# Optimization experiments

Hardware: AMD Instinct MI355X
Metric: run time of the kernel (lower is better)

## Reference

```python
import jax, jax.numpy as jnp
import numpy as np

# Model dims (mamba_ssm defaults: expand=2, d_state=16, d_conv=4, dt_rank=ceil(d_model/16))
V, D_MODEL, N_LAYERS = 32000, 768, 2
D_INNER, D_STATE, D_CONV, DT_RANK = 1536, 16, 4, 48
BATCH, SEQ = 2, 2048


def setup_inputs() -> dict:
    key = jax.random.key(0)
    ks = jax.random.split(key, 10)

    def nrm(k, shape, s=0.02):
        return (jax.random.normal(k, shape) * s).astype(jnp.float32)

    x = jax.random.randint(ks[0], (BATCH, SEQ), 0, V)
    emb = nrm(ks[1], (V, D_MODEL))
    # per-layer Mamba params, stacked on leading layer axis
    W_in = nrm(ks[2], (N_LAYERS, 2 * D_INNER, D_MODEL))          # in_proj (no bias)
    conv_w = nrm(ks[3], (N_LAYERS, D_INNER, 1, D_CONV), 0.1)      # depthwise causal conv
    conv_b = jnp.zeros((N_LAYERS, D_INNER), jnp.float32)
    W_x = nrm(ks[4], (N_LAYERS, DT_RANK + 2 * D_STATE, D_INNER))  # x_proj (no bias)
    W_dt = nrm(ks[5], (N_LAYERS, D_INNER, DT_RANK), 0.05)         # dt_proj
    b_dt = jnp.full((N_LAYERS, D_INNER), -4.0, jnp.float32)       # softplus(-4) ~ small dt
    # A initialized as -exp(A_log) with A_log = log(1..d_state), per mamba_ssm
    A_log = jnp.log(jnp.broadcast_to(
        jnp.arange(1, D_STATE + 1, dtype=jnp.float32), (N_LAYERS, D_INNER, D_STATE)))
    D_skip = jnp.ones((N_LAYERS, D_INNER), jnp.float32)
    W_out = nrm(ks[6], (N_LAYERS, D_MODEL, D_INNER))              # out_proj (no bias)
    ln_g = jnp.ones((D_MODEL,), jnp.float32)
    ln_b = jnp.zeros((D_MODEL,), jnp.float32)
    head_w = nrm(ks[7], (V, D_MODEL))
    head_b = jnp.zeros((V,), jnp.float32)
    return dict(x=x, emb=emb, W_in=W_in, conv_w=conv_w, conv_b=conv_b, W_x=W_x,
                W_dt=W_dt, b_dt=b_dt, A_log=A_log, D_skip=D_skip, W_out=W_out,
                ln_g=ln_g, ln_b=ln_b, head_w=head_w, head_b=head_b)


def mamba_block(h, W_in, conv_w, conv_b, W_x, W_dt, b_dt, A_log, D_skip, W_out):
    # h: (B, L, D_MODEL)
    xz = jnp.einsum('bld,ed->ble', h, W_in)              # (B, L, 2*d_inner)
    u, z = jnp.split(xz, 2, axis=-1)
    # causal depthwise conv over time
    uc = jnp.transpose(u, (0, 2, 1))                     # (B, d_inner, L)
    uc = jax.lax.conv_general_dilated(
        uc, conv_w, window_strides=(1,), padding=[(D_CONV - 1, 0)],
        feature_group_count=D_INNER, dimension_numbers=('NCH', 'OIH', 'NCH'))
    u = jax.nn.silu(jnp.transpose(uc, (0, 2, 1)) + conv_b)
    # input-dependent dt, B, C
    x_dbl = jnp.einsum('bld,ed->ble', u, W_x)            # (B, L, dt_rank+2*d_state)
    dtl, Bm, Cm = jnp.split(x_dbl, [DT_RANK, DT_RANK + D_STATE], axis=-1)
    dt = jax.nn.softplus(jnp.einsum('blr,dr->bld', dtl, W_dt) + b_dt)  # (B, L, d_inner)
    A = -jnp.exp(A_log)                                  # (d_inner, d_state)

    def step(hst, inp):
        dt_t, u_t, B_t, C_t = inp                        # (B,d_inner),(B,d_inner),(B,d_state),(B,d_state)
        hst = jnp.exp(dt_t[..., None] * A) * hst + (dt_t * u_t)[..., None] * B_t[:, None, :]
        y_t = jnp.einsum('bds,bs->bd', hst, C_t)
        return hst, y_t

    h0 = jnp.zeros((u.shape[0], D_INNER, D_STATE), u.dtype)
    xs = (dt.transpose(1, 0, 2), u.transpose(1, 0, 2),
          Bm.transpose(1, 0, 2), Cm.transpose(1, 0, 2))
    _, ys = jax.lax.scan(step, h0, xs)                   # (L, B, d_inner)
    y = ys.transpose(1, 0, 2) + u * D_skip
    y = y * jax.nn.silu(z)
    return jnp.einsum('bli,oi->blo', y, W_out)           # back to (B, L, D_MODEL)


def reference(x, emb, W_in, conv_w, conv_b, W_x, W_dt, b_dt, A_log, D_skip,
              W_out, ln_g, ln_b, head_w, head_b):
    h = emb[x]                                           # (B, L, D_MODEL)
    for l in range(N_LAYERS):
        h = h + mamba_block(h, W_in[l], conv_w[l], conv_b[l], W_x[l], W_dt[l],
                            b_dt[l], A_log[l], D_skip[l], W_out[l])
    mu = jnp.mean(h, axis=-1, keepdims=True)
    var = jnp.mean((h - mu) ** 2, axis=-1, keepdims=True)
    hn = (h - mu) * jax.lax.rsqrt(var + 1e-5) * ln_g + ln_b
    return jnp.einsum('bld,vd->blv', hn, head_w) + head_b
```

## Files before the change

### kernel.cpp

```cpp
#include <hip/hip_runtime.h>
#include <hip/hip_bf16.h>
#include <stdint.h>

#define BL    4096
#define DM    768
#define DI    1536
#define DS    16
#define DCONV 4
#define DTR   48
#define NL    2
#define SEQL  2048
#define BATCH 2
#define VOC   32000
#define NCH   32
#define CT    64

typedef __bf16 bf16_t;
typedef __bf16 bf16x8 __attribute__((ext_vector_type(8)));
typedef __bf16 bf16x4 __attribute__((ext_vector_type(4)));
typedef float  f32x4  __attribute__((ext_vector_type(4)));

__device__ __forceinline__ float sigmoidf_(float x) { return 1.f / (1.f + __expf(-x)); }
__device__ __forceinline__ float softplus_(float x) {
  return (x > 20.f) ? x : log1pf(__expf(x));
}

__global__ __launch_bounds__(256) void k_embed(const int* __restrict__ x,
                                               const float* __restrict__ emb,
                                               float* __restrict__ h,
                                               bf16_t* __restrict__ hb,
                                               bf16_t* __restrict__ dtl) {
  int row = blockIdx.x;
  if (row < 256) {
    int r = row * 16 + (threadIdx.x >> 4);
    dtl[r * 64 + 48 + (threadIdx.x & 15)] = (bf16_t)0.f;
  }
  int tok = x[row];
  const float* e = emb + (size_t)tok * DM;
  float* hr = h + (size_t)row * DM;
  bf16_t* hbr = hb + (size_t)row * DM;
  for (int c = threadIdx.x; c < DM; c += 256) {
    float v = e[c];
    hr[c] = v;
    hbr[c] = (bf16_t)v;
  }
}

#define NV0 1179648L
#define NV1 589824L
#define NV2 6144000L
#define NS3 393216L
#define NS4 196608L
#define NVT (NV0 + NV1 + NV2)
#define NTOT (NVT + NS3 + NS4)

__global__ __launch_bounds__(256) void k_cvtw(const float* __restrict__ Win,
                                              const float* __restrict__ Wout,
                                              const float* __restrict__ Whead,
                                              const float* __restrict__ Wx,
                                              const float* __restrict__ Wdt,
                                              bf16_t* __restrict__ bin,
                                              bf16_t* __restrict__ bout,
                                              bf16_t* __restrict__ bhead,
                                              bf16_t* __restrict__ bx,
                                              bf16_t* __restrict__ bdt) {
  long i = (long)blockIdx.x * 256 + threadIdx.x;
  if (i >= NTOT) return;
  if (i < NVT) {
    const float* s; bf16_t* d; long j = i;
    if (i < NV0)            { s = Win;   d = bin; }
    else if (i < NV0 + NV1) { s = Wout;  d = bout;  j = i - NV0; }
    else                    { s = Whead; d = bhead; j = i - NV0 - NV1; }
    float4 v = ((const float4*)s)[j];
    bf16x4 o;
    o[0] = (bf16_t)v.x; o[1] = (bf16_t)v.y; o[2] = (bf16_t)v.z; o[3] = (bf16_t)v.w;
    ((bf16x4*)d)[j] = o;
  } else if (i < NVT + NS3) {
    long j = i - NVT;
    int l = (int)(j / (128 * 1536));
    int rr = (int)((j / 1536) % 128);
    int c = (int)(j % 1536);
    bx[j] = (bf16_t)(rr < 80 ? Wx[((long)l * 80 + rr) * 1536 + c] : 0.f);
  } else {
    long j = i - NVT - NS3;
    int l = (int)(j / (1536 * 64));
    int r = (int)((j / 64) % 1536);
    int c = (int)(j & 63);
    bdt[j] = (bf16_t)(c < DTR ? Wdt[((long)l * 1536 + r) * DTR + c] : 0.f);
  }
}

__global__ __launch_bounds__(256) void k_conv(const float* __restrict__ xz,
                                              const float* __restrict__ cw,
                                              const float* __restrict__ cb,
                                              bf16_t* __restrict__ ucb, long total) {
  long i = (long)blockIdx.x * 256 + threadIdx.x;
  if (i >= total) return;
  int d = (int)(i % DI);
  long row = i / DI;
  int l = (int)(row % SEQL);
  const float* w = cw + (size_t)d * DCONV;
  float s = cb[d];
#pragma unroll
  for (int j = 0; j < DCONV; j++) {
    int lj = l - (DCONV - 1) + j;
    if (lj >= 0) s += xz[(row - (DCONV - 1) + j) * (2 * DI) + d] * w[j];
  }
  float v = s * sigmoidf_(s);
  ucb[i] = (bf16_t)v;
}

__global__ __launch_bounds__(256) void k_xfin(const float* __restrict__ xp,
                                              float* __restrict__ xdbl,
                                              bf16_t* __restrict__ dtl) {
  long i = (long)blockIdx.x * 256 + threadIdx.x;
  if (i >= (long)BL * 80) return;
  float s = xp[i] + xp[i + (long)BL * 80] + xp[i + 2L * BL * 80] + xp[i + 3L * BL * 80];
  xdbl[i] = s;
  int row = (int)(i / 80), col = (int)(i % 80);
  if (col < DTR) dtl[(long)row * 64 + col] = (bf16_t)s;
}

__global__ __launch_bounds__(256) void k_scan1(const bf16_t* __restrict__ dt,
                                               const bf16_t* __restrict__ uc,
                                               const float* __restrict__ xdbl,
                                               const float* __restrict__ A_log,
                                               float* __restrict__ cA,
                                               float* __restrict__ cB) {
  int gi = blockIdx.x * 256 + threadIdx.x;
  int s = gi & 15;
  int rest = gi >> 4;
  int d = rest % DI;
  int rest2 = rest / DI;
  int c = rest2 % NCH;
  int b = rest2 / NCH;
  float a = -__expf(A_log[d * DS + s]);
  long l0 = (long)c * CT;
  const bf16_t* dtp = dt + ((long)b * SEQL + l0) * DI + d;
  const bf16_t* ucp = uc + ((long)b * SEQL + l0) * DI + d;
  const float*  Bp  = xdbl + ((long)b * SEQL + l0) * 80 + DTR + s;
  float S = 0.f, hh = 0.f;
#pragma unroll 4
  for (int l = 0; l < CT; l++) {
    float dtv = (float)dtp[(long)l * DI];
    float uv  = (float)ucp[(long)l * DI];
    float Bv  = Bp[(long)l * 80];
    S += dtv;
    hh = __expf(dtv * a) * hh + (dtv * uv) * Bv;
  }
  cA[gi] = __expf(a * S);
  cB[gi] = hh;
}

__global__ __launch_bounds__(256) void k_scan2(const float* __restrict__ cA,
                                               const float* __restrict__ cB,
                                               float* __restrict__ hst) {
  int gj = blockIdx.x * 256 + threadIdx.x;
  int ds_ = gj & (DI * DS - 1);
  int b = gj / (DI * DS);
  float h = 0.f;
#pragma unroll
  for (int c = 0; c < NCH; c++) {
    long idx = ((long)(b * NCH + c) * DI * DS) + ds_;
    hst[idx] = h;
    h = cA[idx] * h + cB[idx];
  }
}

__global__ __launch_bounds__(256) void k_scan3g(const bf16_t* __restrict__ dt,
                                                const bf16_t* uc,
                                                const float* __restrict__ xdbl,
                                                const float* __restrict__ A_log,
                                                const float* __restrict__ hst,
                                                const float* __restrict__ xz,
                                                const float* __restrict__ Dsk,
                                                bf16_t* o) {
  int gi = blockIdx.x * 256 + threadIdx.x;
  int s = gi & 15;
  int rest = gi >> 4;
  int d = rest % DI;
  int rest2 = rest / DI;
  int c = rest2 % NCH;
  int b = rest2 / NCH;
  float a = -__expf(A_log[d * DS + s]);
  float dval = Dsk[d];
  long l0 = (long)c * CT;
  const bf16_t* dtp = dt + ((long)b * SEQL + l0) * DI + d;
  const bf16_t* ucp = uc + ((long)b * SEQL + l0) * DI + d;
  const float*  Bp  = xdbl + ((long)b * SEQL + l0) * 80 + DTR + s;
  const float*  Cp  = Bp + DS;
  const float*  zp  = xz + ((long)b * SEQL + l0) * (2 * DI) + DI + d;
  bf16_t* yp = o + ((long)b * SEQL + l0) * DI + d;
  float h = hst[gi];
#pragma unroll 4
  for (int l = 0; l < CT; l++) {
    float dtv = (float)dtp[(long)l * DI];
    float uv  = (float)ucp[(long)l * DI];
    float Bv  = Bp[(long)l * 80];
    float Cv  = Cp[(long)l * 80];
    h = __expf(dtv * a) * h + (dtv * uv) * Bv;
    float y = h * Cv;
    y += __shfl_xor(y, 1);
    y += __shfl_xor(y, 2);
    y += __shfl_xor(y, 4);
    y += __shfl_xor(y, 8);
    if (s == 0) {
      float z = zp[(long)l * 2 * DI];
      float yy = (y + uv * dval) * z * sigmoidf_(z);
      yp[(long)l * DI] = (bf16_t)yy;
    }
  }
}

__global__ __launch_bounds__(256) void k_ln(const float* __restrict__ h,
                                            const float* __restrict__ g,
                                            const float* __restrict__ bta,
                                            bf16_t* __restrict__ o) {
  __shared__ float sm[4];
  int row = blockIdx.x;
  int t = threadIdx.x;
  const float* hr = h + (long)row * DM;
  float v0 = hr[t], v1 = hr[t + 256], v2 = hr[t + 512];
  float s = v0 + v1 + v2;
#pragma unroll
  for (int off = 32; off > 0; off >>= 1) s += __shfl_down(s, off);
  if ((t & 63) == 0) sm[t >> 6] = s;
  __syncthreads();
  float mu = (sm[0] + sm[1] + sm[2] + sm[3]) * (1.f / DM);
  __syncthreads();
  float d0 = v0 - mu, d1 = v1 - mu, d2 = v2 - mu;
  float q = d0 * d0 + d1 * d1 + d2 * d2;
#pragma unroll
  for (int off = 32; off > 0; off >>= 1) q += __shfl_down(q, off);
  if ((t & 63) == 0) sm[t >> 6] = q;
  __syncthreads();
  float var = (sm[0] + sm[1] + sm[2] + sm[3]) * (1.f / DM);
  float rs = rsqrtf(var + 1e-5f);
  bf16_t* orow = o + (long)row * DM;
  orow[t]       = (bf16_t)(d0 * rs * g[t]       + bta[t]);
  orow[t + 256] = (bf16_t)(d1 * rs * g[t + 256] + bta[t + 256]);
  orow[t + 512] = (bf16_t)(d2 * rs * g[t + 512] + bta[t + 512]);
}

__device__ __forceinline__ void stage16(const bf16_t* gp, bf16_t* lp) {
  __builtin_amdgcn_global_load_lds(
      (const __attribute__((address_space(1))) uint32_t*)gp,
      (__attribute__((address_space(3))) uint32_t*)lp, 16, 0, 0);
}

#define WAITV8()  asm volatile("s_waitcnt vmcnt(8)" ::: "memory")
#define WAITV0()  asm volatile("s_waitcnt vmcnt(0)" ::: "memory")
#define BARRIER() do { __builtin_amdgcn_s_barrier();                            \
                       asm volatile("" ::: "memory"); } while (0)

#define GLD256(ab, j, ktt, pp) do {                                             \
    int idx_ = (j) * 512 + tid;                                                 \
    int r_ = idx_ >> 3; int c16_ = idx_ & 7;                                    \
    size_t col_ = (size_t)(ktt) * 64 + (size_t)((c16_ ^ (r_ & 7)) << 3);        \
    const bf16_t* gp_ = (ab) ? (Wp + ((size_t)(n0 + r_)) * K + col_)            \
                             : (Ap + ((size_t)(m0 + r_)) * K + col_);           \
    bf16_t* lp_ = lds + ((((pp) * 2 + (ab)) * 256 + r_) * 64) + c16_ * 8;       \
    stage16(gp_, lp_);                                                          \
  } while (0)

#define STAGE256(pp, ktt) do {                                                  \
    GLD256(0, 0, ktt, pp); GLD256(0, 1, ktt, pp);                               \
    GLD256(0, 2, ktt, pp); GLD256(0, 3, ktt, pp);                               \
    GLD256(1, 0, ktt, pp); GLD256(1, 1, ktt, pp);                               \
    GLD256(1, 2, ktt, pp); GLD256(1, 3, ktt, pp);                               \
  } while (0)

#define COMPUTE_KH(pp, kh) do {                                                 \
    const char* lb_ = (const char*)lds;                                         \
    bf16x8 bfr_[4];                                                             \
    _Pragma("unroll") for (int f = 0; f < 4; ++f) {                             \
      int row_ = wn * 64 + f * 16 + fr;                                         \
      int byte_ = (((pp) * 2 + 1) * 256 + row_) * 128 +                         \
                  (((kh) * 64 + kq * 16) ^ ((row_ & 7) << 4));                  \
      bfr_[f] = *(const bf16x8*)(lb_ + byte_);                                  \
    }                                                                           \
    _Pragma("unroll") for (int mg = 0; mg < 2; ++mg) {                          \
      bf16x8 afr_[4];                                                           \
      _Pragma("unroll") for (int f = 0; f < 4; ++f) {                           \
        int row_ = wm * 128 + mg * 64 + f * 16 + fr;                            \
        int byte_ = (((pp) * 2 + 0) * 256 + row_) * 128 +                       \
                    (((kh) * 64 + kq * 16) ^ ((row_ & 7) << 4));                \
        afr_[f] = *(const bf16x8*)(lb_ + byte_);                                \
      }                                                                         \
      __builtin_amdgcn_s_setprio(1);                                            \
      _Pragma("unroll") for (int fm = 0; fm < 4; ++fm)                          \
        _Pragma("unroll") for (int fn = 0; fn < 4; ++fn)                        \
          acc[mg * 4 + fm][fn] = __builtin_amdgcn_mfma_f32_16x16x32_bf16(       \
              afr_[fm], bfr_[fn], acc[mg * 4 + fm][fn], 0, 0, 0);               \
      __builtin_amdgcn_s_setprio(0);                                            \
    }                                                                           \
  } while (0)

template <int EPI>
__global__ __launch_bounds__(512, 2) void k_gemm256(const bf16_t* __restrict__ Ap,
                                                    const bf16_t* __restrict__ Wp,
                                                    float* __restrict__ C,
                                                    const float* __restrict__ bias,
                                                    int K, int ldc) {
  __shared__ bf16_t lds[2 * 2 * 256 * 64];
  const int tid = threadIdx.x;
  const int lane = tid & 63;
  const int wid = tid >> 6;
  const int wm = wid >> 2, wn = wid & 3;
  const int fr = lane & 15, kq = lane >> 4;

  const int cpx = gridDim.x >> 3;
  const int wg = ((int)blockIdx.x & 7) * cpx + ((int)blockIdx.x >> 3);
  const long m0 = (long)(wg & 15) * 256;
  const long n0 = (long)(wg >> 4) * 256;

  f32x4 acc[8][4];
#pragma unroll
  for (int i = 0; i < 8; i++)
#pragma unroll
    for (int j = 0; j < 4; j++) acc[i][j] = (f32x4){0.f, 0.f, 0.f, 0.f};

  STAGE256(0, 0);
  const int NT = K >> 6;
  for (int kt = 0; kt < NT; ++kt) {
    const int p = kt & 1;
    const bool pre = (kt + 1 < NT);
    if (pre) STAGE256(p ^ 1, kt + 1);
    if (pre) WAITV8(); else WAITV0();
    BARRIER();
    COMPUTE_KH(p, 0);
    COMPUTE_KH(p, 1);
    BARRIER();
  }

  {
    float* lf = (float*)(void*)lds;
    const int q = lane >> 4;
    const int cc = lane & 15;
    float4 bias4 = {0.f, 0.f, 0.f, 0.f};
    if (EPI == 1) bias4 = *(const float4*)&bias[n0 + lane * 4];
#pragma unroll
    for (int p = 0; p < 4; ++p) {
      __syncthreads();
      if (wm == (p >> 1)) {
        const int mgb = (p & 1) * 4;
#pragma unroll
        for (int m4 = 0; m4 < 4; ++m4)
#pragma unroll
          for (int n = 0; n < 4; ++n) {
            f32x4 v = acc[mgb + m4][n];
            float* dst = &lf[(m4 * 16 + q * 4) * 260 + wn * 64 + n * 16 + cc];
#pragma unroll
            for (int r = 0; r < 4; ++r) dst[r * 260] = v[r];
          }
      }
      __syncthreads();
      const long rowg0 = m0 + p * 64;
#pragma unroll
      for (int it = 0; it < 8; ++it) {
        int row_loc = wid * 8 + it;
        f32x4 v = *(const f32x4*)&lf[row_loc * 260 + lane * 4];
        float* gp = &C[(rowg0 + row_loc) * (long)ldc + n0 + lane * 4];
        if (EPI == 1) {
          v[0] += bias4.x; v[1] += bias4.y; v[2] += bias4.z; v[3] += bias4.w;
          __builtin_nontemporal_store(v, (f32x4*)gp);
        } else {
          *(f32x4*)gp = v;
        }
      }
    }
  }
}

#define GLD128(ab, j, ktt, pp) do {                                             \
    int idx_ = (j) * 256 + tid;                                                 \
    int r_ = idx_ >> 3; int c16_ = idx_ & 7;                                    \
    size_t col_ = kb + (size_t)(ktt) * 64 + (size_t)((c16_ ^ (r_ & 7)) << 3);   \
    const bf16_t* gp_ = (ab) ? (Wp + ((size_t)(n0 + r_)) * K + col_)            \
                             : (Ap + ((size_t)(m0 + r_)) * K + col_);           \
    bf16_t* lp_ = lds + ((((pp) * 2 + (ab)) * 128 + r_) * 64) + c16_ * 8;       \
    stage16(gp_, lp_);                                                          \
  } while (0)

#define STAGE128(pp, ktt) do {                                                  \
    GLD128(0, 0, ktt, pp); GLD128(0, 1, ktt, pp);                               \
    GLD128(0, 2, ktt, pp); GLD128(0, 3, ktt, pp);                               \
    GLD128(1, 0, ktt, pp); GLD128(1, 1, ktt, pp);                               \
    GLD128(1, 2, ktt, pp); GLD128(1, 3, ktt, pp);                               \
  } while (0)

#define COMPUTE128(pp, kh) do {                                                 \
    const char* lb_ = (const char*)lds;                                         \
    bf16x8 af_[4], bv_[4];                                                      \
    _Pragma("unroll") for (int f = 0; f < 4; ++f) {                             \
      int row_ = wn * 64 + f * 16 + fr;                                         \
      int byte_ = (((pp) * 2 + 1) * 128 + row_) * 128 +                         \
                  (((kh) * 64 + kq * 16) ^ ((row_ & 7) << 4));                  \
      bv_[f] = *(const bf16x8*)(lb_ + byte_);                                   \
    }                                                                           \
    _Pragma("unroll") for (int f = 0; f < 4; ++f) {                             \
      int row_ = wm * 64 + f * 16 + fr;                                         \
      int byte_ = (((pp) * 2 + 0) * 128 + row_) * 128 +                         \
                  (((kh) * 64 + kq * 16) ^ ((row_ & 7) << 4));                  \
      af_[f] = *(const bf16x8*)(lb_ + byte_);                                   \
    }                                                                           \
    __builtin_amdgcn_s_setprio(1);                                              \
    _Pragma("unroll") for (int fm = 0; fm < 4; ++fm)                            \
      _Pragma("unroll") for (int fn = 0; fn < 4; ++fn)                          \
        acc[fm][fn] = __builtin_amdgcn_mfma_f32_16x16x32_bf16(                  \
            af_[fm], bv_[fn], acc[fm][fn], 0, 0, 0);                            \
    __builtin_amdgcn_s_setprio(0);                                              \
  } while (0)

template <int EPI>
__global__ __launch_bounds__(256, 2) void k_gemm128(const bf16_t* __restrict__ Ap,
                                                    const bf16_t* __restrict__ Wp,
                                                    float* __restrict__ C,
                                                    const float* __restrict__ bias,
                                                    bf16_t* __restrict__ side,
                                                    int K, int Ksl, int ldc) {
  __shared__ bf16_t lds[2 * 2 * 128 * 64];
  const int tid = threadIdx.x;
  const int lane = tid & 63;
  const int wv = tid >> 6;
  const int wm = wv >> 1, wn = wv & 1;
  const int fr = lane & 15, kq = lane >> 4;
  const size_t kb = (size_t)blockIdx.y * Ksl;

  const int cpx = gridDim.x >> 3;
  const int wg = ((int)blockIdx.x & 7) * cpx + ((int)blockIdx.x >> 3);
  const long m0 = (long)(wg & 31) * 128;
  const long n0 = (long)(wg >> 5) * 128;

  f32x4 acc[4][4];
#pragma unroll
  for (int i = 0; i < 4; i++)
#pragma unroll
    for (int j = 0; j < 4; j++) acc[i][j] = (f32x4){0.f, 0.f, 0.f, 0.f};

  STAGE128(0, 0);
  const int NT = Ksl >> 6;
  for (int kt = 0; kt < NT; ++kt) {
    const int p = kt & 1;
    const bool pre = (kt + 1 < NT);
    if (pre) STAGE128(p ^ 1, kt + 1);
    if (pre) WAITV8(); else WAITV0();
    BARRIER();
    COMPUTE128(p, 0);
    COMPUTE128(p, 1);
    BARRIER();
  }

  if (EPI == 7) {
    float* Cs = C + (size_t)blockIdx.y * (size_t)BL * 80;
    const int r4 = (lane >> 4) * 4;
    const int cc = lane & 15;
#pragma unroll
    for (int fm = 0; fm < 4; fm++) {
      long rowb = m0 + wm * 64 + fm * 16 + r4;
#pragma unroll
      for (int fn = 0; fn < 4; fn++) {
        long col = n0 + wn * 64 + fn * 16 + cc;
        if (col < 80) {
#pragma unroll
          for (int r = 0; r < 4; r++)
            Cs[(rowb + r) * 80 + col] = acc[fm][fn][r];
        }
      }
    }
    return;
  }

  {
    float* lf = (float*)(void*)lds;
    const int q = lane >> 4;
    const int cc = lane & 15;
    const int colt = (tid & 31) * 4;
    float4 bias4 = {0.f, 0.f, 0.f, 0.f};
    if (EPI == 4) bias4 = *(const float4*)&bias[n0 + colt];
#pragma unroll
    for (int p = 0; p < 4; ++p) {
      __syncthreads();
      if (wm == (p >> 1)) {
#pragma unroll
        for (int fl = 0; fl < 2; ++fl) {
          int fm = (p & 1) * 2 + fl;
#pragma unroll
          for (int fn = 0; fn < 4; ++fn) {
            f32x4 v = acc[fm][fn];
            float* dst = &lf[(fl * 16 + q * 4) * 132 + wn * 64 + fn * 16 + cc];
#pragma unroll
            for (int r = 0; r < 4; ++r) dst[r * 132] = v[r];
          }
        }
      }
      __syncthreads();
      const long rowg0 = m0 + p * 32;
#pragma unroll
      for (int it = 0; it < 4; ++it) {
        int rl = it * 8 + (tid >> 5);
        f32x4 v = *(const f32x4*)&lf[rl * 132 + colt];
        long row = rowg0 + rl;
        long cg = n0 + colt;
        if (EPI == 4) {
          bf16x4 s4;
          s4[0] = (bf16_t)softplus_(v[0] + bias4.x);
          s4[1] = (bf16_t)softplus_(v[1] + bias4.y);
          s4[2] = (bf16_t)softplus_(v[2] + bias4.z);
          s4[3] = (bf16_t)softplus_(v[3] + bias4.w);
          *(bf16x4*)&side[row * (long)ldc + cg] = s4;
        } else {
          float* gp = &C[row * (long)ldc + cg];
          f32x4 c0 = *(const f32x4*)gp;
          v[0] += c0[0]; v[1] += c0[1]; v[2] += c0[2]; v[3] += c0[3];
          *(f32x4*)gp = v;
          bf16x4 s4;
          s4[0] = (bf16_t)v[0]; s4[1] = (bf16_t)v[1];
          s4[2] = (bf16_t)v[2]; s4[3] = (bf16_t)v[3];
          *(bf16x4*)&side[row * (long)ldc + cg] = s4;
        }
      }
    }
  }
}

static inline int cdiv_l(long a, long b) { return (int)((a + b - 1) / b); }

extern "C" void kernel_launch(void* const* d_in, const int* in_sizes, int n_in,
                              void* d_out, int out_size, void* d_ws, size_t ws_size,
                              hipStream_t stream) {
  (void)in_sizes; (void)n_in; (void)out_size; (void)ws_size;
  const int*   x      = (const int*)  d_in[0];
  const float* emb    = (const float*)d_in[1];
  const float* W_in   = (const float*)d_in[2];
  const float* conv_w = (const float*)d_in[3];
  const float* conv_b = (const float*)d_in[4];
  const float* W_x    = (const float*)d_in[5];
  const float* W_dt   = (const float*)d_in[6];
  const float* b_dt   = (const float*)d_in[7];
  const float* A_log  = (const float*)d_in[8];
  const float* D_skip = (const float*)d_in[9];
  const float* W_out  = (const float*)d_in[10];
  const float* ln_g   = (const float*)d_in[11];
  const float* ln_b   = (const float*)d_in[12];
  const float* head_w = (const float*)d_in[13];
  const float* head_b = (const float*)d_in[14];
  float* out = (float*)d_out;

  bf16_t* abuf   = (bf16_t*)d_ws;
  bf16_t* hbf    = abuf   + (size_t)BL * DI;
  bf16_t* dtl    = hbf    + (size_t)BL * DM;
  bf16_t* wb_in  = dtl    + (size_t)BL * 64;
  bf16_t* wb_out = wb_in  + (size_t)2 * 3072 * 768;
  bf16_t* wb_hd  = wb_out + (size_t)2 * 768 * 1536;
  bf16_t* wb_x   = wb_hd  + (size_t)VOC * DM;
  bf16_t* wb_dt  = wb_x   + (size_t)2 * 128 * 1536;

  float*  xz    = out;
  float*  xdbl  = xz    + (size_t)BL * 2 * DI;
  float*  dtb_f = xdbl  + (size_t)BL * 80;
  bf16_t* dtbb  = (bf16_t*)dtb_f;
  float*  h     = dtb_f + (size_t)BL * DI;
  float*  cA    = h     + (size_t)BL * DM;
  float*  cB    = cA    + (size_t)BATCH * NCH * DI * DS;
  float*  hst   = cB    + (size_t)BATCH * NCH * DI * DS;
  float*  xpart = hst   + (size_t)BATCH * DI * DS;

  const int scan_blocks = BATCH * NCH * DI * DS / 256;
  const int st_blocks   = BATCH * DI * DS / 256;

  k_cvtw<<<cdiv_l(NTOT, 256), 256, 0, stream>>>(W_in, W_out, head_w, W_x, W_dt,
                                                wb_in, wb_out, wb_hd, wb_x, wb_dt);
  k_embed<<<BL, 256, 0, stream>>>(x, emb, h, hbf, dtl);

  for (int l = 0; l < NL; ++l) {
    k_gemm256<0><<<(BL / 256) * (2 * DI / 256), 512, 0, stream>>>(
        hbf, wb_in + (size_t)l * 3072 * 768, xz, nullptr, DM, 2 * DI);
    k_conv<<<cdiv_l((long)BL * DI, 256), 256, 0, stream>>>(
        xz, conv_w + (size_t)l * DI * DCONV, conv_b + (size_t)l * DI,
        abuf, (long)BL * DI);
    k_gemm128<7><<<dim3(32, 4), 256, 0, stream>>>(
        abuf, wb_x + (size_t)l * 128 * 1536, xpart, nullptr, nullptr,
        DI, DI / 4, 80);
    k_xfin<<<cdiv_l((long)BL * 80, 256), 256, 0, stream>>>(xpart, xdbl, dtl);
    k_gemm128<4><<<(BL / 128) * (DI / 128), 256, 0, stream>>>(
        dtl, wb_dt + (size_t)l * 1536 * 64, nullptr, b_dt + (size_t)l * DI, dtbb,
        64, 64, DI);
    k_scan1<<<scan_blocks, 256, 0, stream>>>(dtbb, abuf, xdbl,
                                             A_log + (size_t)l * DI * DS, cA, cB);
    k_scan2<<<st_blocks, 256, 0, stream>>>(cA, cB, hst);
    k_scan3g<<<scan_blocks, 256, 0, stream>>>(dtbb, abuf, xdbl,
                                              A_log + (size_t)l * DI * DS, hst,
                                              xz, D_skip + (size_t)l * DI, abuf);
    k_gemm128<5><<<(BL / 128) * (DM / 128), 256, 0, stream>>>(
        abuf, wb_out + (size_t)l * 768 * 1536, h, nullptr, hbf, DI, DI, DM);
  }

  k_ln<<<BL, 256, 0, stream>>>(h, ln_g, ln_b, abuf);
  k_gemm256<1><<<(BL / 256) * (VOC / 256), 512, 0, stream>>>(
      abuf, wb_hd, out, head_b, DM, VOC);
}
```

Before: 974.7 us.

## Use three-stage K=32 LDS pipeline with packed row layout in 256x256 GEMM

```diff
diff --git a/kernel.cpp b/kernel.cpp
--- a/kernel.cpp
+++ b/kernel.cpp
@@ -249,60 +249,59 @@
 }
 
 #define WAITV8()  asm volatile("s_waitcnt vmcnt(8)" ::: "memory")
+#define WAITV4()  asm volatile("s_waitcnt vmcnt(4)" ::: "memory")
 #define WAITV0()  asm volatile("s_waitcnt vmcnt(0)" ::: "memory")
 #define BARRIER() do { __builtin_amdgcn_s_barrier();                            \
                        asm volatile("" ::: "memory"); } while (0)
 
+
 #define GLD256(ab, j, ktt, pp) do {                                             \
-    int idx_ = (j) * 512 + tid;                                                 \
-    int r_ = idx_ >> 3; int c16_ = idx_ & 7;                                    \
-    size_t col_ = (size_t)(ktt) * 64 + (size_t)((c16_ ^ (r_ & 7)) << 3);        \
+    int L_ = (j) * 512 + tid;                          \
+    int rowp_ = L_ >> 3;                                            \
+    int chs_ = L_ & 7;                                                          \
+    int chl_ = chs_ ^ (rowp_ & 7);                                              \
+    int r_ = rowp_ * 2 + (chl_ >> 2);                                           \
+    size_t col_ = (size_t)(ktt) * 32 + (size_t)((chl_ & 3) * 8);                \
     const bf16_t* gp_ = (ab) ? (Wp + ((size_t)(n0 + r_)) * K + col_)            \
                              : (Ap + ((size_t)(m0 + r_)) * K + col_);           \
-    bf16_t* lp_ = lds + ((((pp) * 2 + (ab)) * 256 + r_) * 64) + c16_ * 8;       \
+    bf16_t* lp_ = lds + ((((pp) * 2 + (ab)) * 128 + rowp_) * 64) + chs_ * 8;    \
     stage16(gp_, lp_);                                                          \
   } while (0)
 
 #define STAGE256(pp, ktt) do {                                                  \
     GLD256(0, 0, ktt, pp); GLD256(0, 1, ktt, pp);                               \
-    GLD256(0, 2, ktt, pp); GLD256(0, 3, ktt, pp);                               \
     GLD256(1, 0, ktt, pp); GLD256(1, 1, ktt, pp);                               \
-    GLD256(1, 2, ktt, pp); GLD256(1, 3, ktt, pp);                               \
   } while (0)
 
-#define COMPUTE_KH(pp, kh) do {                                                 \
+#define FRAG_BYTE(ab, pp, row_)                                                 \
+    ((((pp) * 2 + (ab)) * 128 + ((row_) >> 1)) * 128 +                          \
+     (((((row_) & 1) * 4 + kq) ^ (((row_) >> 1) & 7)) * 16))
+
+#define COMPUTE256(pp) do {                                                     \
     const char* lb_ = (const char*)lds;                                         \
     bf16x8 bfr_[4];                                                             \
     _Pragma("unroll") for (int f = 0; f < 4; ++f) {                             \
       int row_ = wn * 64 + f * 16 + fr;                                         \
-      int byte_ = (((pp) * 2 + 1) * 256 + row_) * 128 +                         \
-                  (((kh) * 64 + kq * 16) ^ ((row_ & 7) << 4));                  \
-      bfr_[f] = *(const bf16x8*)(lb_ + byte_);                                  \
+      bfr_[f] = *(const bf16x8*)(lb_ + FRAG_BYTE(1, pp, row_));                 \
     }                                                                           \
-    _Pragma("unroll") for (int mg = 0; mg < 2; ++mg) {                          \
-      bf16x8 afr_[4];                                                           \
-      _Pragma("unroll") for (int f = 0; f < 4; ++f) {                           \
-        int row_ = wm * 128 + mg * 64 + f * 16 + fr;                            \
-        int byte_ = (((pp) * 2 + 0) * 256 + row_) * 128 +                       \
-                    (((kh) * 64 + kq * 16) ^ ((row_ & 7) << 4));                \
-        afr_[f] = *(const bf16x8*)(lb_ + byte_);                                \
-      }                                                                         \
+    _Pragma("unroll") for (int fm = 0; fm < 8; ++fm) {                          \
+      int row_ = wm * 128 + fm * 16 + fr;                                       \
+      bf16x8 af_ = *(const bf16x8*)(lb_ + FRAG_BYTE(0, pp, row_));              \
       __builtin_amdgcn_s_setprio(1);                                            \
-      _Pragma("unroll") for (int fm = 0; fm < 4; ++fm)                          \
-        _Pragma("unroll") for (int fn = 0; fn < 4; ++fn)                        \
-          acc[mg * 4 + fm][fn] = __builtin_amdgcn_mfma_f32_16x16x32_bf16(       \
-              afr_[fm], bfr_[fn], acc[mg * 4 + fm][fn], 0, 0, 0);               \
+      _Pragma("unroll") for (int fn = 0; fn < 4; ++fn)                          \
+        acc[fm][fn] = __builtin_amdgcn_mfma_f32_16x16x32_bf16(                  \
+            af_, bfr_[fn], acc[fm][fn], 0, 0, 0);                               \
       __builtin_amdgcn_s_setprio(0);                                            \
     }                                                                           \
   } while (0)
 
 template <int EPI>
-__global__ __launch_bounds__(512, 2) void k_gemm256(const bf16_t* __restrict__ Ap,
+__global__ __launch_bounds__(512, 1) void k_gemm256(const bf16_t* __restrict__ Ap,
                                                     const bf16_t* __restrict__ Wp,
                                                     float* __restrict__ C,
                                                     const float* __restrict__ bias,
                                                     int K, int ldc) {
-  __shared__ bf16_t lds[2 * 2 * 256 * 64];
+  __shared__ bf16_t lds[3 * 2 * 128 * 64];
   const int tid = threadIdx.x;
   const int lane = tid & 63;
   const int wid = tid >> 6;
@@ -321,16 +320,23 @@
     for (int j = 0; j < 4; j++) acc[i][j] = (f32x4){0.f, 0.f, 0.f, 0.f};
 
   STAGE256(0, 0);
-  const int NT = K >> 6;
+  STAGE256(1, 1);
+  const int NT = K >> 5;
+  int p = 0;
   for (int kt = 0; kt < NT; ++kt) {
-    const int p = kt & 1;
-    const bool pre = (kt + 1 < NT);
-    if (pre) STAGE256(p ^ 1, kt + 1);
-    if (pre) WAITV8(); else WAITV0();
+    if (kt + 2 < NT) {
+      int p2 = p + 2; if (p2 >= 3) p2 -= 3;
+      STAGE256(p2, kt + 2);
+      WAITV8();
+    } else if (kt + 1 < NT) {
+      WAITV4();
+    } else {
+      WAITV0();
+    }
     BARRIER();
-    COMPUTE_KH(p, 0);
-    COMPUTE_KH(p, 1);
+    COMPUTE256(p);
     BARRIER();
+    if (++p >= 3) p -= 3;
   }
 
   {
@@ -340,10 +346,10 @@
     float4 bias4 = {0.f, 0.f, 0.f, 0.f};
     if (EPI == 1) bias4 = *(const float4*)&bias[n0 + lane * 4];
 #pragma unroll
-    for (int p = 0; p < 4; ++p) {
+    for (int pp = 0; pp < 4; ++pp) {
       __syncthreads();
-      if (wm == (p >> 1)) {
-        const int mgb = (p & 1) * 4;
+      if (wm == (pp >> 1)) {
+        const int mgb = (pp & 1) * 4;
 #pragma unroll
         for (int m4 = 0; m4 < 4; ++m4)
 #pragma unroll
@@ -355,7 +361,7 @@
           }
       }
       __syncthreads();
-      const long rowg0 = m0 + p * 64;
+      const long rowg0 = m0 + pp * 64;
 #pragma unroll
       for (int it = 0; it < 8; ++it) {
         int row_loc = wid * 8 + it;
@@ -371,6 +377,8 @@
     }
   }
 }
+
+#define WAITV8B() asm volatile("s_waitcnt vmcnt(8)" ::: "memory")
 
 #define GLD128(ab, j, ktt, pp) do {                                             \
     int idx_ = (j) * 256 + tid;                                                 \
@@ -444,7 +452,7 @@
     const int p = kt & 1;
     const bool pre = (kt + 1 < NT);
     if (pre) STAGE128(p ^ 1, kt + 1);
-    if (pre) WAITV8(); else WAITV0();
+    if (pre) WAITV8B(); else WAITV0();
     BARRIER();
     COMPUTE128(p, 0);
     COMPUTE128(p, 1);
```

Measured after the change: 1.016 ms. 4.2% more time.
